# Optimization experiments

Hardware: AMD Instinct MI355X
Metric: run time of the kernel (lower is better)

Reference implementation:

```python
import jax, jax.numpy as jnp
import numpy as np

RATE = 0.999  # moving_average_rate
EPS_NORM = 1e-12
EPS_CNT = 1e-6


def l2norm(v, axis=-1):
    # matches torch F.normalize(dim=axis) with default eps
    n = jnp.sqrt(jnp.sum(v * v, axis=axis, keepdims=True))
    return v / jnp.maximum(n, EPS_NORM)


def setup_inputs() -> dict:
    key = jax.random.key(0)
    ks = jax.random.split(key, 7)
    b, c, h, w, k = 8, 256, 64, 64, 2048
    x = jax.random.normal(ks[0], (b, c, h, w), dtype=jnp.float32)
    y = jax.random.uniform(ks[1], (b, 4, h, w), dtype=jnp.float32)
    feat_w = jax.random.normal(ks[2], (k, c + 4), dtype=jnp.float32) * 0.02
    w1 = jax.random.normal(ks[3], (c + 4, c), dtype=jnp.float32) * 0.02
    b1 = jnp.zeros((c,), dtype=jnp.float32)
    w2 = jax.random.normal(ks[4], (c, c), dtype=jnp.float32) * 0.02
    b2 = jnp.zeros((c,), dtype=jnp.float32)
    return {"x": x, "y": y, "feat_w": feat_w, "w1": w1, "b1": b1, "w2": w2, "b2": b2}


def reference(x, y, feat_w, w1, b1, w2, b2):
    b, c, h, w = x.shape
    k = feat_w.shape[0]
    # flatten spatial: (n, c) with n = b*h*w
    x_flat = jnp.transpose(x, (0, 2, 3, 1)).reshape(-1, c)
    y_flat = jnp.transpose(y, (0, 2, 3, 1)).reshape(-1, 4)

    # cosine-similarity scores against codebook features (no grad in original)
    xn = l2norm(x_flat)                       # (n, c)
    mn = l2norm(feat_w[:, :-4])               # (k, c)
    score = xn @ mn.T                         # (n, k)

    # top1 EMA codebook update
    xy = jnp.concatenate([x_flat, y_flat], axis=1)          # (n, c+4)
    ind = jnp.argmax(score, axis=1)                          # (n,)
    counts = jax.ops.segment_sum(jnp.ones_like(ind, jnp.float32), ind, num_segments=k)  # (k,)
    sums = jax.ops.segment_sum(xy, ind, num_segments=k)      # (k, c+4)
    embed_mean = sums / (counts[:, None] + EPS_CNT)          # (k, c+4)
    new_w = feat_w * RATE + embed_mean * (1.0 - RATE)        # (k, c+4)

    # softmax attention over (updated) normalized codebook
    p = jax.nn.softmax(score, axis=1)                        # (n, k)
    out = p @ l2norm(new_w)                                  # (n, c+4)

    # MLP: Linear -> GELU -> Linear (drop=0)
    out = jax.nn.gelu(out @ w1 + b1) @ w2 + b2               # (n, c)
    return jnp.transpose(out.reshape(b, h, w, c), (0, 3, 1, 2))
```

## Files before the change

kernel.cpp:

```cpp
#include <hip/hip_runtime.h>
#include <cstdint>
#include <cstddef>


typedef short v8s __attribute__((ext_vector_type(8)));
typedef float v4f __attribute__((ext_vector_type(4)));

__device__ __forceinline__ unsigned short f2b(float f) {
  unsigned u = __float_as_uint(f);
  u = (u + 0x7FFFu + ((u >> 16) & 1u)) >> 16;
  return (unsigned short)u;
}
__device__ __forceinline__ float b2f(short s) {
  return __uint_as_float((unsigned)(unsigned short)s << 16);
}
__device__ __forceinline__ float gelu_t(float x) {
  float x3 = x * x * x;
  return 0.5f * x * (1.0f + tanhf(0.7978845608028654f * (x + 0.044715f * x3)));
}
__device__ __forceinline__ float gelu_fast(float x) {
  float u = 0.7978845608028654f * (x + 0.044715f * x * x * x);
  float tt = __expf(2.0f * u);
  return x * tt * __builtin_amdgcn_rcpf(tt + 1.0f);
}
__device__ __forceinline__ unsigned int mono(float f) {
  unsigned u = __float_as_uint(f);
  return (u & 0x80000000u) ? ~u : (u | 0x80000000u);
}
__device__ __forceinline__ void async16(const short* g, short* l) {
  __builtin_amdgcn_global_load_lds(
      (const __attribute__((address_space(1))) unsigned int*)g,
      (__attribute__((address_space(3))) unsigned int*)l, 16, 0, 0);
}

__global__ void transpose_norm_kernel(const float* __restrict__ x, short* __restrict__ xn,
                                      float* __restrict__ norms) {
  __shared__ float tile[32 * 257];
  __shared__ float part[8][32];
  __shared__ float invn[32];
  int t = threadIdx.x, bx = blockIdx.x;
  int b = bx >> 7, st = bx & 127;
  int s0 = st * 32;
  int sl = t & 31, cp = t >> 5;
  const float* xb = x + (size_t)b * 256 * 4096 + s0 + sl;
  float ss = 0.f;
#pragma unroll 4
  for (int i = 0; i < 32; ++i) {
    int c = cp * 32 + i;
    float v = xb[(size_t)c * 4096];
    tile[sl * 257 + c] = v;
    ss += v * v;
  }
  part[cp][sl] = ss;
  __syncthreads();
  if (t < 32) {
    float tot = 0.f;
#pragma unroll
    for (int p = 0; p < 8; ++p) tot += part[p][t];
    float nrm = fmaxf(sqrtf(tot), 1e-12f);
    invn[t] = 1.0f / nrm;
    norms[(size_t)b * 4096 + s0 + t] = nrm;
  }
  __syncthreads();
  size_t obase = ((size_t)b * 4096 + s0) * 256 + t;
  for (int s = 0; s < 32; ++s)
    xn[obase + (size_t)s * 256] = (short)f2b(tile[s * 257 + t] * invn[s]);
}

__global__ void cbnorm_kernel(const float* __restrict__ fw, short* __restrict__ mn) {
  int t = threadIdx.x;
  int wv = t >> 6, l = t & 63;
  int r = blockIdx.x * 4 + wv;
  const float* row = fw + (size_t)r * 260;
  float v[4]; float ss = 0.f;
#pragma unroll
  for (int p = 0; p < 4; ++p) { v[p] = row[l + p * 64]; ss += v[p] * v[p]; }
#pragma unroll
  for (int m = 1; m < 64; m <<= 1) ss += __shfl_xor(ss, m, 64);
  float inv = 1.0f / fmaxf(sqrtf(ss), 1e-12f);
#pragma unroll
  for (int p = 0; p < 4; ++p) mn[(size_t)r * 256 + l + p * 64] = (short)f2b(v[p] * inv);
}

template <int KTOT, int LDA, int LDB>
__device__ __forceinline__ void gemm_core2(const short* __restrict__ A, const short* __restrict__ B,
                                           int mt, int nt, int t, v4f acc[4][4],
                                           short* smem) {
  short* As = smem;
  short* Bs = smem + 4096;
  const int l = t & 63, w = t >> 6;
  const int wm = w >> 1, wn = w & 1;
  const int lane16 = l & 15, q4 = l >> 4;
#pragma unroll
  for (int i = 0; i < 4; ++i)
#pragma unroll
    for (int j = 0; j < 4; ++j)
#pragma unroll
      for (int r = 0; r < 4; ++r) acc[i][j][r] = 0.0f;
  const int srow = (w << 5) + (l >> 2);
  const int scol = (l & 3) << 3;
  const short* ga = A + (size_t)(mt * 128 + srow) * LDA + scol;
  const short* gb = B + (size_t)(nt * 128 + srow) * LDB + scol;
  short* la = As + (w << 5) * 32;
  short* lb = Bs + (w << 5) * 32;
  int kk = 0;
  for (; kk + 64 <= KTOT; kk += 64) {
    async16(ga + kk, la);
    async16(ga + (size_t)16 * LDA + kk, la + 512);
    async16(gb + kk, lb);
    async16(gb + (size_t)16 * LDB + kk, lb + 512);
    async16(ga + kk + 32, la + 8192);
    async16(ga + (size_t)16 * LDA + kk + 32, la + 8704);
    async16(gb + kk + 32, lb + 8192);
    async16(gb + (size_t)16 * LDB + kk + 32, lb + 8704);
    __syncthreads();
    v8s af[4], bf[4];
#pragma unroll
    for (int i = 0; i < 4; ++i) af[i] = *(const v8s*)&As[(wm * 64 + i * 16 + lane16) * 32 + q4 * 8];
#pragma unroll
    for (int j = 0; j < 4; ++j) bf[j] = *(const v8s*)&Bs[(wn * 64 + j * 16 + lane16) * 32 + q4 * 8];
#pragma unroll
    for (int i = 0; i < 4; ++i)
#pragma unroll
      for (int j = 0; j < 4; ++j)
        acc[i][j] = __builtin_amdgcn_mfma_f32_16x16x32_bf16(af[i], bf[j], acc[i][j], 0, 0, 0);
#pragma unroll
    for (int i = 0; i < 4; ++i) af[i] = *(const v8s*)&As[8192 + (wm * 64 + i * 16 + lane16) * 32 + q4 * 8];
#pragma unroll
    for (int j = 0; j < 4; ++j) bf[j] = *(const v8s*)&Bs[8192 + (wn * 64 + j * 16 + lane16) * 32 + q4 * 8];
#pragma unroll
    for (int i = 0; i < 4; ++i)
#pragma unroll
      for (int j = 0; j < 4; ++j)
        acc[i][j] = __builtin_amdgcn_mfma_f32_16x16x32_bf16(af[i], bf[j], acc[i][j], 0, 0, 0);
    __syncthreads();
  }
  if (kk < KTOT) {
    async16(ga + kk, la);
    async16(ga + (size_t)16 * LDA + kk, la + 512);
    async16(gb + kk, lb);
    async16(gb + (size_t)16 * LDB + kk, lb + 512);
    __syncthreads();
    v8s af[4], bf[4];
#pragma unroll
    for (int i = 0; i < 4; ++i) af[i] = *(const v8s*)&As[(wm * 64 + i * 16 + lane16) * 32 + q4 * 8];
#pragma unroll
    for (int j = 0; j < 4; ++j) bf[j] = *(const v8s*)&Bs[(wn * 64 + j * 16 + lane16) * 32 + q4 * 8];
#pragma unroll
    for (int i = 0; i < 4; ++i)
#pragma unroll
      for (int j = 0; j < 4; ++j)
        acc[i][j] = __builtin_amdgcn_mfma_f32_16x16x32_bf16(af[i], bf[j], acc[i][j], 0, 0, 0);
    __syncthreads();
  }
}

#define CP 136

__global__ __launch_bounds__(256, 2) void gemm1_kernel(const short* __restrict__ A, const short* __restrict__ B,
                                                       short* __restrict__ Q,
                                                       unsigned long long* __restrict__ packed_part,
                                                       float* __restrict__ lrow_part) {
  __shared__ __align__(16) short smem[18432];
  __shared__ unsigned long long partk[128][2];
  __shared__ float partq[128][2];
  int t = threadIdx.x, bx = blockIdx.x;
  int nt = bx >> 8, mt = bx & 255;
  v4f acc[4][4];
  gemm_core2<256, 256, 256>(A, B, mt, nt, t, acc, smem);
  int l = t & 63, w = t >> 6, wm = w >> 1, wn = w & 1, lane16 = l & 15, q4 = l >> 4;
  int rowbase = mt * 128, colbase = nt * 128;
#pragma unroll
  for (int i = 0; i < 4; ++i) {
#pragma unroll
    for (int r = 0; r < 4; ++r) {
      int lr = wm * 64 + i * 16 + q4 * 4 + r;
      float qs = 0.f;
      unsigned long long best = 0ull;
#pragma unroll
      for (int j = 0; j < 4; ++j) {
        float s = acc[i][j][r];
        int col_l = wn * 64 + j * 16 + lane16;
        float qv = __expf(s) - 1.0f;
        smem[lr * CP + col_l] = (short)f2b(qv);
        qs += qv;
        unsigned long long key = ((unsigned long long)mono(s) << 32) |
                                 (unsigned long long)(unsigned int)(~(unsigned)(colbase + col_l));
        if (key > best) best = key;
      }
#pragma unroll
      for (int m = 1; m < 16; m <<= 1) {
        unsigned long long ob = __shfl_xor(best, m, 64);
        if (ob > best) best = ob;
        qs += __shfl_xor(qs, m, 64);
      }
      if (lane16 == 0) { partk[lr][wn] = best; partq[lr][wn] = qs; }
    }
  }
  __syncthreads();
  if (t < 128) {
    unsigned long long b0 = partk[t][0], b1 = partk[t][1];
    packed_part[((size_t)nt << 15) + rowbase + t] = (b1 > b0) ? b1 : b0;
    lrow_part[((size_t)nt << 15) + rowbase + t] = partq[t][0] + partq[t][1];
  }
#pragma unroll
  for (int k2 = 0; k2 < 8; ++k2) {
    int idx = k2 * 256 + t;
    int row = idx >> 4, c8 = (idx & 15) * 8;
    *(v8s*)&Q[(size_t)(rowbase + row) * 2048 + colbase + c8] =
        *(const v8s*)&smem[row * CP + c8];
  }
}

__global__ void ind_kernel(const unsigned long long* __restrict__ packed_part,
                           const float* __restrict__ lrow_part,
                           int* __restrict__ ind, float* __restrict__ lrow,
                           float* __restrict__ cnt) {
  int i = blockIdx.x * 256 + threadIdx.x;
  unsigned long long best = 0ull;
  float ls = 0.f;
#pragma unroll
  for (int nt = 0; nt < 16; ++nt) {
    unsigned long long v = packed_part[((size_t)nt << 15) + i];
    if (v > best) best = v;
    ls += lrow_part[((size_t)nt << 15) + i];
  }
  int id = (int)(~(unsigned int)(best & 0xFFFFFFFFull));
  ind[i] = id;
  lrow[i] = ls;
  atomicAdd(&cnt[id], 1.0f);
}

__global__ void scan_kernel(const float* __restrict__ cnt, int* __restrict__ offs,
                            int* __restrict__ cursor) {
  __shared__ int part[256];
  int t = threadIdx.x;
  int local[8]; int s = 0;
#pragma unroll
  for (int i = 0; i < 8; ++i) { local[i] = s; s += (int)cnt[t * 8 + i]; }
  part[t] = s;
  __syncthreads();
  for (int off = 1; off < 256; off <<= 1) {
    int v = (t >= off) ? part[t - off] : 0;
    __syncthreads();
    part[t] += v;
    __syncthreads();
  }
  int base = (t > 0) ? part[t - 1] : 0;
#pragma unroll
  for (int i = 0; i < 8; ++i) {
    int o = base + local[i];
    offs[t * 8 + i] = o;
    cursor[t * 8 + i] = o;
  }
  if (t == 255) offs[2048] = part[255];
}

__global__ void fill_kernel(const int* __restrict__ ind, int* __restrict__ cursor,
                            int* __restrict__ sorted) {
  int i = blockIdx.x * 256 + threadIdx.x;
  int id = ind[i];
  int pos = atomicAdd(&cursor[id], 1);
  sorted[pos] = i;
}

__global__ void segsum_kernel(const short* __restrict__ xn, const float* __restrict__ norms,
                              const float* __restrict__ y, const int* __restrict__ offs,
                              const int* __restrict__ sorted, float* __restrict__ sums) {
  int r = blockIdx.x, t = threadIdx.x;
  int beg = offs[r], end = offs[r + 1];
  float a0 = 0.f, a1 = 0.f;
  for (int j = beg; j < end; ++j) {
    int node = sorted[j];
    float nm = norms[node];
    a0 += b2f(xn[(size_t)node * 256 + t]) * nm;
    if (t < 4) {
      int b = node >> 12, s = node & 4095;
      a1 += y[(size_t)b * 16384 + t * 4096 + s];
    }
  }
  sums[(size_t)r * 260 + t] = a0;
  if (t < 4) sums[(size_t)r * 260 + 256 + t] = a1;
}

__global__ void neww_kernel(const float* __restrict__ fw, const float* __restrict__ sums,
                            const float* __restrict__ cnt, short* __restrict__ nwt,
                            float* __restrict__ colsum) {
  int r = blockIdx.x;
  int l = threadIdx.x;
  float cv = cnt[r] + 1e-6f;
  float vals[5]; float ss = 0.f;
#pragma unroll
  for (int p = 0; p < 5; ++p) {
    int c = l + p * 64;
    float v = 0.f;
    if (c < 260) {
      float m = sums[(size_t)r * 260 + c] / cv;
      v = fw[(size_t)r * 260 + c] * 0.999f + m * 0.001f;
    }
    vals[p] = v; ss += v * v;
  }
#pragma unroll
  for (int m = 1; m < 64; m <<= 1) ss += __shfl_xor(ss, m, 64);
  float inv = 1.0f / fmaxf(sqrtf(ss), 1e-12f);
#pragma unroll
  for (int p = 0; p < 5; ++p) {
    int c = l + p * 64;
    if (c < 260) {
      float v = vals[p] * inv;
      nwt[(size_t)c * 2048 + r] = (short)f2b(v);
      atomicAdd(&colsum[c], v);
    }
  }
}

__global__ void const_kernel(const float* __restrict__ colsum, const float* __restrict__ w1,
                             const float* __restrict__ b1, const float* __restrict__ w2,
                             const float* __restrict__ b2, float* __restrict__ c0,
                             float* __restrict__ zc, float* __restrict__ hc,
                             float* __restrict__ oc) {
  __shared__ float c0s[260], hcs[256];
  int t = threadIdx.x;
  for (int c = t; c < 260; c += 256) {
    float v = colsum[c] * (1.0f / 2048.0f);
    c0s[c] = v; c0[c] = v;
  }
  __syncthreads();
  float z = b1[t];
  for (int i = 0; i < 260; ++i) z = fmaf(c0s[i], w1[(size_t)i * 256 + t], z);
  float h = gelu_t(z);
  zc[t] = z; hc[t] = h; hcs[t] = h;
  __syncthreads();
  float o = b2[t];
  for (int i = 0; i < 256; ++i) o = fmaf(hcs[i], w2[(size_t)i * 256 + t], o);
  oc[t] = o;
}

__global__ void wtrans_kernel(const float* __restrict__ w1, const float* __restrict__ w2,
                              short* __restrict__ w1t, short* __restrict__ w2t) {
  int j = blockIdx.x;
  int t = threadIdx.x;
  if (j < 256) {
    for (int i = t; i < 288; i += 64)
      w1t[(size_t)j * 288 + i] = (short)f2b(i < 260 ? w1[(size_t)i * 256 + j] : 0.0f);
  } else {
    int jj = j - 256;
    for (int i = t; i < 256; i += 64)
      w2t[(size_t)jj * 256 + i] = (short)f2b(w2[(size_t)i * 256 + jj]);
  }
}

__global__ __launch_bounds__(256, 2) void gemm2_kernel(const short* __restrict__ A, const short* __restrict__ B,
                                                       const float* __restrict__ lrow,
                                                       const float* __restrict__ colsum,
                                                       const float* __restrict__ c0,
                                                       short* __restrict__ D) {
  __shared__ __align__(16) short smem[18432];
  int t = threadIdx.x, bx = blockIdx.x;
  int nt = bx >> 8, mt = bx & 255;
  v4f acc[4][4];
  gemm_core2<2048, 2048, 2048>(A, B, mt, nt, t, acc, smem);
  int l = t & 63, w = t >> 6, wm = w >> 1, wn = w & 1, lane16 = l & 15, q4 = l >> 4;
  int rowbase = mt * 128, colbase = nt * 128;
#pragma unroll
  for (int i = 0; i < 4; ++i) {
#pragma unroll
    for (int r = 0; r < 4; ++r) {
      int lr = wm * 64 + i * 16 + q4 * 4 + r;
      float linv = 1.0f / (2048.0f + lrow[rowbase + lr]);
#pragma unroll
      for (int j = 0; j < 4; ++j) {
        int col_l = wn * 64 + j * 16 + lane16;
        int col_g = colbase + col_l;
        float v = 0.0f;
        if (col_g < 260)
          v = (colsum[col_g] + acc[i][j][r]) * linv - c0[col_g];
        smem[lr * CP + col_l] = (short)f2b(v);
      }
    }
  }
  __syncthreads();
#pragma unroll
  for (int k2 = 0; k2 < 8; ++k2) {
    int idx = k2 * 256 + t;
    int row = idx >> 4, c8 = (idx & 15) * 8;
    int cc = colbase + c8;
    if (cc < 288)
      *(v8s*)&D[(size_t)(rowbase + row) * 288 + cc] =
          *(const v8s*)&smem[row * CP + c8];
  }
}

__global__ __launch_bounds__(256, 2) void gemm3_kernel(const short* __restrict__ A, const short* __restrict__ B,
                                                       const float* __restrict__ zc,
                                                       const float* __restrict__ hc,
                                                       short* __restrict__ E) {
  __shared__ __align__(16) short smem[18432];
  int t = threadIdx.x, bx = blockIdx.x;
  int nt = bx >> 8, mt = bx & 255;
  v4f acc[4][4];
  gemm_core2<288, 288, 288>(A, B, mt, nt, t, acc, smem);
  int l = t & 63, w = t >> 6, wm = w >> 1, wn = w & 1, lane16 = l & 15, q4 = l >> 4;
  int rowbase = mt * 128, colbase = nt * 128;
#pragma unroll
  for (int i = 0; i < 4; ++i)
#pragma unroll
    for (int r = 0; r < 4; ++r) {
      int lr = wm * 64 + i * 16 + q4 * 4 + r;
#pragma unroll
      for (int j = 0; j < 4; ++j) {
        int col_l = wn * 64 + j * 16 + lane16;
        int col_g = colbase + col_l;
        float z = zc[col_g] + acc[i][j][r];
        smem[lr * CP + col_l] = (short)f2b(gelu_fast(z) - hc[col_g]);
      }
    }
  __syncthreads();
#pragma unroll
  for (int k2 = 0; k2 < 8; ++k2) {
    int idx = k2 * 256 + t;
    int row = idx >> 4, c8 = (idx & 15) * 8;
    *(v8s*)&E[(size_t)(rowbase + row) * 256 + colbase + c8] =
        *(const v8s*)&smem[row * CP + c8];
  }
}

__global__ __launch_bounds__(256, 2) void gemm4_kernel(const short* __restrict__ A, const short* __restrict__ B,
                                                       const float* __restrict__ oc,
                                                       float* __restrict__ out) {
  __shared__ __align__(16) short smem[18432];
  float* F = (float*)smem;
  int t = threadIdx.x, bx = blockIdx.x;
  int nt = bx >> 8, mt = bx & 255;
  v4f acc[4][4];
  gemm_core2<256, 256, 256>(A, B, mt, nt, t, acc, smem);
  int l = t & 63, w = t >> 6, wm = w >> 1, wn = w & 1, lane16 = l & 15, q4 = l >> 4;
  int b_ = mt >> 5;
  int sbase = (mt & 31) * 128;
  for (int q = 0; q < 4; ++q) {
    __syncthreads();
    if (wn == (q >> 1)) {
#pragma unroll
      for (int i = 0; i < 4; ++i)
#pragma unroll
        for (int r = 0; r < 4; ++r) {
          int srow = wm * 64 + i * 16 + q4 * 4 + r;
#pragma unroll
          for (int jj = 0; jj < 2; ++jj) {
            int j = (q & 1) * 2 + jj;
            int c_in = jj * 16 + lane16;
            int col_g = nt * 128 + q * 32 + c_in;
            F[c_in * 132 + srow] = oc[col_g] + acc[i][j][r];
          }
        }
    }
    __syncthreads();
#pragma unroll
    for (int k2 = 0; k2 < 4; ++k2) {
      int idx = k2 * 256 + t;
      int c_loc = idx >> 5, s4 = (idx & 31) * 4;
      v4f vv = *(const v4f*)&F[c_loc * 132 + s4];
      int cg = nt * 128 + q * 32 + c_loc;
      *(v4f*)&out[(size_t)b_ * 1048576 + (size_t)cg * 4096 + sbase + s4] = vv;
    }
  }
}

extern "C" void kernel_launch(void* const* d_in, const int* in_sizes, int n_in,
                              void* d_out, int out_size, void* d_ws, size_t ws_size,
                              hipStream_t stream) {
  const float* x  = (const float*)d_in[0];
  const float* y  = (const float*)d_in[1];
  const float* fw = (const float*)d_in[2];
  const float* w1 = (const float*)d_in[3];
  const float* b1 = (const float*)d_in[4];
  const float* w2 = (const float*)d_in[5];
  const float* b2 = (const float*)d_in[6];
  float* out = (float*)d_out;
  char* ws = (char*)d_ws;

  short* qbuf = (short*)(ws + 0);
  short* xn   = (short*)(ws + 134217728);
  short* ebuf = xn;
  short* mn   = (short*)(ws + 150994944);
  float* lrow = (float*)(ws + 152305664);
  int*   ind  = (int*)(ws + 152436736);
  float* cnt  = (float*)(ws + 152567808);
  float* sums = (float*)(ws + 152576000);
  float* lrow_part = (float*)(ws + 152576000);
  short* nwt  = (short*)(ws + 154705920);
  float* colsum = (float*)(ws + 156278784);
  float* c0   = (float*)(ws + 156279936);
  float* zc   = (float*)(ws + 156281088);
  float* hc   = (float*)(ws + 156282112);
  float* oc   = (float*)(ws + 156283136);
  short* w1t  = (short*)(ws + 156284160);
  short* w2t  = (short*)(ws + 156431616);
  short* dbuf = (short*)(ws + 156562688);
  float* norms  = (float*)(ws + 156562688);
  int*   offs   = (int*)(ws + 156693760);
  int*   cursor = (int*)(ws + 156702464);
  int*   sorted = (int*)(ws + 156710656);
  unsigned long long* packed_part =
      (unsigned long long*)(ws + 156841728);
  if (ws_size < 175437056ull) return;

  hipMemsetAsync(cnt,    0, 8192, stream);
  hipMemsetAsync(nwt,    0, 1572864, stream);
  hipMemsetAsync(colsum, 0, 1152, stream);

  transpose_norm_kernel<<<1024, 256, 0, stream>>>(x, xn, norms);
  cbnorm_kernel<<<512, 256, 0, stream>>>(fw, mn);
  gemm1_kernel<<<4096, 256, 0, stream>>>(xn, mn, qbuf, packed_part, lrow_part);
  ind_kernel<<<128, 256, 0, stream>>>(packed_part, lrow_part, ind, lrow, cnt);
  scan_kernel<<<1, 256, 0, stream>>>(cnt, offs, cursor);
  fill_kernel<<<128, 256, 0, stream>>>(ind, cursor, sorted);
  segsum_kernel<<<2048, 256, 0, stream>>>(xn, norms, y, offs, sorted, sums);
  neww_kernel<<<2048, 64, 0, stream>>>(fw, sums, cnt, nwt, colsum);
  const_kernel<<<1, 256, 0, stream>>>(colsum, w1, b1, w2, b2, c0, zc, hc, oc);
  wtrans_kernel<<<512, 64, 0, stream>>>(w1, w2, w1t, w2t);
  gemm2_kernel<<<768, 256, 0, stream>>>(qbuf, nwt, lrow, colsum, c0, dbuf);
  gemm3_kernel<<<512, 256, 0, stream>>>(dbuf, w1t, zc, hc, ebuf);
  gemm4_kernel<<<512, 256, 0, stream>>>(ebuf, w2t, oc, out);
}
```

Baseline: 403.9 us.

## Fuse score recompute, exp and P@V into flash-style attention kernel

gemm1 is cut down to computing only the per-row argmax keys, so it no longer writes the 128MB bf16 exp-score matrix or row sums. A new attn_kernel recomputes the score tiles per 64-row block, applies exp-1, accumulates row sums, and multiplies by the updated codebook in registers, replacing gemm2's read of the Q buffer. This trades the large HBM write and read for doing the first GEMM twice. It also adds lower occupancy and a serial loop over 16 column tiles with several barriers per step.

```diff
diff --git a/kernel.cpp b/kernel.cpp
--- a/kernel.cpp
+++ b/kernel.cpp
@@ -157,13 +157,10 @@
 
 #define CP 136
 
-__global__ __launch_bounds__(256, 2) void gemm1_kernel(const short* __restrict__ A, const short* __restrict__ B,
-                                                       short* __restrict__ Q,
-                                                       unsigned long long* __restrict__ packed_part,
-                                                       float* __restrict__ lrow_part) {
-  __shared__ __align__(16) short smem[18432];
+__global__ __launch_bounds__(256, 4) void gemm1_kernel(const short* __restrict__ A, const short* __restrict__ B,
+                                                       unsigned long long* __restrict__ packed_part) {
+  __shared__ __align__(16) short smem[16384];
   __shared__ unsigned long long partk[128][2];
-  __shared__ float partq[128][2];
   int t = threadIdx.x, bx = blockIdx.x;
   int nt = bx >> 8, mt = bx & 255;
   v4f acc[4][4];
@@ -175,59 +172,41 @@
 #pragma unroll
     for (int r = 0; r < 4; ++r) {
       int lr = wm * 64 + i * 16 + q4 * 4 + r;
-      float qs = 0.f;
       unsigned long long best = 0ull;
 #pragma unroll
       for (int j = 0; j < 4; ++j) {
         float s = acc[i][j][r];
-        int col_l = wn * 64 + j * 16 + lane16;
-        float qv = __expf(s) - 1.0f;
-        smem[lr * CP + col_l] = (short)f2b(qv);
-        qs += qv;
+        int col_g = colbase + wn * 64 + j * 16 + lane16;
         unsigned long long key = ((unsigned long long)mono(s) << 32) |
-                                 (unsigned long long)(unsigned int)(~(unsigned)(colbase + col_l));
+                                 (unsigned long long)(unsigned int)(~(unsigned)col_g);
         if (key > best) best = key;
       }
 #pragma unroll
       for (int m = 1; m < 16; m <<= 1) {
         unsigned long long ob = __shfl_xor(best, m, 64);
         if (ob > best) best = ob;
-        qs += __shfl_xor(qs, m, 64);
-      }
-      if (lane16 == 0) { partk[lr][wn] = best; partq[lr][wn] = qs; }
+      }
+      if (lane16 == 0) partk[lr][wn] = best;
     }
   }
   __syncthreads();
   if (t < 128) {
     unsigned long long b0 = partk[t][0], b1 = partk[t][1];
     packed_part[((size_t)nt << 15) + rowbase + t] = (b1 > b0) ? b1 : b0;
-    lrow_part[((size_t)nt << 15) + rowbase + t] = partq[t][0] + partq[t][1];
-  }
-#pragma unroll
-  for (int k2 = 0; k2 < 8; ++k2) {
-    int idx = k2 * 256 + t;
-    int row = idx >> 4, c8 = (idx & 15) * 8;
-    *(v8s*)&Q[(size_t)(rowbase + row) * 2048 + colbase + c8] =
-        *(const v8s*)&smem[row * CP + c8];
   }
 }
 
 __global__ void ind_kernel(const unsigned long long* __restrict__ packed_part,
-                           const float* __restrict__ lrow_part,
-                           int* __restrict__ ind, float* __restrict__ lrow,
-                           float* __restrict__ cnt) {
+                           int* __restrict__ ind, float* __restrict__ cnt) {
   int i = blockIdx.x * 256 + threadIdx.x;
   unsigned long long best = 0ull;
-  float ls = 0.f;
 #pragma unroll
   for (int nt = 0; nt < 16; ++nt) {
     unsigned long long v = packed_part[((size_t)nt << 15) + i];
     if (v > best) best = v;
-    ls += lrow_part[((size_t)nt << 15) + i];
   }
   int id = (int)(~(unsigned int)(best & 0xFFFFFFFFull));
   ind[i] = id;
-  lrow[i] = ls;
   atomicAdd(&cnt[id], 1.0f);
 }
 
@@ -350,44 +329,141 @@
   }
 }
 
-__global__ __launch_bounds__(256, 2) void gemm2_kernel(const short* __restrict__ A, const short* __restrict__ B,
-                                                       const float* __restrict__ lrow,
-                                                       const float* __restrict__ colsum,
-                                                       const float* __restrict__ c0,
-                                                       short* __restrict__ D) {
-  __shared__ __align__(16) short smem[18432];
-  int t = threadIdx.x, bx = blockIdx.x;
-  int nt = bx >> 8, mt = bx & 255;
-  v4f acc[4][4];
-  gemm_core2<2048, 2048, 2048>(A, B, mt, nt, t, acc, smem);
-  int l = t & 63, w = t >> 6, wm = w >> 1, wn = w & 1, lane16 = l & 15, q4 = l >> 4;
-  int rowbase = mt * 128, colbase = nt * 128;
-#pragma unroll
-  for (int i = 0; i < 4; ++i) {
+__global__ __launch_bounds__(256, 2) void attn_kernel(const short* __restrict__ xn,
+                                                      const short* __restrict__ mn,
+                                                      const short* __restrict__ nwt,
+                                                      const float* __restrict__ colsum,
+                                                      const float* __restrict__ c0,
+                                                      short* __restrict__ D) {
+  __shared__ __align__(16) short smem[32768];
+  __shared__ float lsum[64];
+  int t = threadIdx.x, mt = blockIdx.x;
+  int l = t & 63, w = t >> 6;
+  int lane16 = l & 15, q4 = l >> 4;
+  if (t < 64) lsum[t] = 0.f;
+  v4f acc_o[4][5];
+#pragma unroll
+  for (int rt = 0; rt < 4; ++rt)
+#pragma unroll
+    for (int j = 0; j < 5; ++j)
+#pragma unroll
+      for (int r = 0; r < 4; ++r) acc_o[rt][j][r] = 0.0f;
+  float qs_acc[4][4];
+#pragma unroll
+  for (int rt = 0; rt < 4; ++rt)
+#pragma unroll
+    for (int r = 0; r < 4; ++r) qs_acc[rt][r] = 0.0f;
+  const int lrow4 = l >> 2, lc8 = (l & 3) << 3;
+
+  for (int nt = 0; nt < 16; ++nt) {
+    __syncthreads();
+    v4f acc_s[4][2];
+#pragma unroll
+    for (int rt = 0; rt < 4; ++rt)
+#pragma unroll
+      for (int ct = 0; ct < 2; ++ct)
+#pragma unroll
+        for (int r = 0; r < 4; ++r) acc_s[rt][ct][r] = 0.0f;
+    for (int kh = 0; kh < 2; ++kh) {
+#pragma unroll
+      for (int s = 0; s < 4; ++s)
+        async16(xn + (size_t)(mt * 64 + s * 16 + lrow4) * 256 + kh * 128 + w * 32 + lc8,
+                &smem[w * 2048 + s * 512]);
+#pragma unroll
+      for (int s = 0; s < 8; ++s)
+        async16(mn + (size_t)(nt * 128 + s * 16 + lrow4) * 256 + kh * 128 + w * 32 + lc8,
+                &smem[8192 + w * 4096 + s * 512]);
+      __syncthreads();
+#pragma unroll
+      for (int ks = 0; ks < 4; ++ks) {
+        v8s a[4], b[2];
+#pragma unroll
+        for (int rt = 0; rt < 4; ++rt)
+          a[rt] = *(const v8s*)&smem[ks * 2048 + rt * 512 + lane16 * 32 + q4 * 8];
+#pragma unroll
+        for (int ct = 0; ct < 2; ++ct)
+          b[ct] = *(const v8s*)&smem[8192 + ks * 4096 + (2 * w + ct) * 512 + lane16 * 32 + q4 * 8];
+#pragma unroll
+        for (int rt = 0; rt < 4; ++rt)
+#pragma unroll
+          for (int ct = 0; ct < 2; ++ct)
+            acc_s[rt][ct] = __builtin_amdgcn_mfma_f32_16x16x32_bf16(a[rt], b[ct], acc_s[rt][ct], 0, 0, 0);
+      }
+      __syncthreads();
+    }
+#pragma unroll
+    for (int rt = 0; rt < 4; ++rt)
+#pragma unroll
+      for (int ct = 0; ct < 2; ++ct)
+#pragma unroll
+        for (int r = 0; r < 4; ++r) {
+          float qv = __expf(acc_s[rt][ct][r]) - 1.0f;
+          qs_acc[rt][r] += qv;
+          smem[24576 + w * 2048 + rt * 512 + (q4 * 4 + r) * 32 + ct * 16 + lane16] = (short)f2b(qv);
+        }
+    __syncthreads();
+    for (int h = 0; h < 2; ++h) {
+      int idbase = w * 10;
+#pragma unroll
+      for (int u = 0; u < 10; ++u) {
+        int id = idbase + u;
+        int ks2 = (id >= 20) ? 1 : 0;
+        int slab = id - ks2 * 20;
+        async16(nwt + (size_t)(slab * 16 + lrow4) * 2048 + nt * 128 + h * 64 + ks2 * 32 + lc8,
+                &smem[ks2 * 10240 + slab * 512]);
+      }
+      __syncthreads();
+#pragma unroll
+      for (int ks2 = 0; ks2 < 2; ++ks2) {
+        int kg = h * 2 + ks2;
+        v8s a[4], b[5];
+#pragma unroll
+        for (int rt = 0; rt < 4; ++rt)
+          a[rt] = *(const v8s*)&smem[24576 + kg * 2048 + rt * 512 + lane16 * 32 + q4 * 8];
+#pragma unroll
+        for (int j = 0; j < 5; ++j)
+          b[j] = *(const v8s*)&smem[ks2 * 10240 + (w * 5 + j) * 512 + lane16 * 32 + q4 * 8];
+#pragma unroll
+        for (int rt = 0; rt < 4; ++rt)
+#pragma unroll
+          for (int j = 0; j < 5; ++j)
+            acc_o[rt][j] = __builtin_amdgcn_mfma_f32_16x16x32_bf16(a[rt], b[j], acc_o[rt][j], 0, 0, 0);
+      }
+      __syncthreads();
+    }
+  }
+#pragma unroll
+  for (int rt = 0; rt < 4; ++rt)
 #pragma unroll
     for (int r = 0; r < 4; ++r) {
-      int lr = wm * 64 + i * 16 + q4 * 4 + r;
-      float linv = 1.0f / (2048.0f + lrow[rowbase + lr]);
-#pragma unroll
-      for (int j = 0; j < 4; ++j) {
-        int col_l = wn * 64 + j * 16 + lane16;
-        int col_g = colbase + col_l;
-        float v = 0.0f;
-        if (col_g < 260)
-          v = (colsum[col_g] + acc[i][j][r]) * linv - c0[col_g];
-        smem[lr * CP + col_l] = (short)f2b(v);
-      }
-    }
-  }
-  __syncthreads();
-#pragma unroll
-  for (int k2 = 0; k2 < 8; ++k2) {
+      float v = qs_acc[rt][r];
+#pragma unroll
+      for (int m = 1; m < 16; m <<= 1) v += __shfl_xor(v, m, 64);
+      if (lane16 == 0) atomicAdd(&lsum[rt * 16 + q4 * 4 + r], v);
+    }
+  __syncthreads();
+#pragma unroll
+  for (int rt = 0; rt < 4; ++rt)
+#pragma unroll
+    for (int r = 0; r < 4; ++r) {
+      int m = rt * 16 + q4 * 4 + r;
+      float linv = 1.0f / (2048.0f + lsum[m]);
+#pragma unroll
+      for (int j = 0; j < 5; ++j) {
+        int c = w * 80 + j * 16 + lane16;
+        if (c < 288) {
+          float v = 0.0f;
+          if (c < 260) v = (colsum[c] + acc_o[rt][j][r]) * linv - c0[c];
+          smem[m * 296 + c] = (short)f2b(v);
+        }
+      }
+    }
+  __syncthreads();
+#pragma unroll
+  for (int k2 = 0; k2 < 9; ++k2) {
     int idx = k2 * 256 + t;
-    int row = idx >> 4, c8 = (idx & 15) * 8;
-    int cc = colbase + c8;
-    if (cc < 288)
-      *(v8s*)&D[(size_t)(rowbase + row) * 288 + cc] =
-          *(const v8s*)&smem[row * CP + c8];
+    int row = idx / 36, ch = idx - row * 36;
+    *(v8s*)&D[(size_t)(mt * 64 + row) * 288 + ch * 8] = *(const v8s*)&smem[row * 296 + ch * 8];
   }
 }
 
@@ -479,31 +555,28 @@
   float* out = (float*)d_out;
   char* ws = (char*)d_ws;
 
-  short* qbuf = (short*)(ws + 0);
-  short* xn   = (short*)(ws + 134217728);
-  short* ebuf = xn;
-  short* mn   = (short*)(ws + 150994944);
-  float* lrow = (float*)(ws + 152305664);
-  int*   ind  = (int*)(ws + 152436736);
-  float* cnt  = (float*)(ws + 152567808);
-  float* sums = (float*)(ws + 152576000);
-  float* lrow_part = (float*)(ws + 152576000);
-  short* nwt  = (short*)(ws + 154705920);
-  float* colsum = (float*)(ws + 156278784);
-  float* c0   = (float*)(ws + 156279936);
-  float* zc   = (float*)(ws + 156281088);
-  float* hc   = (float*)(ws + 156282112);
-  float* oc   = (float*)(ws + 156283136);
-  short* w1t  = (short*)(ws + 156284160);
-  short* w2t  = (short*)(ws + 156431616);
-  short* dbuf = (short*)(ws + 156562688);
-  float* norms  = (float*)(ws + 156562688);
-  int*   offs   = (int*)(ws + 156693760);
-  int*   cursor = (int*)(ws + 156702464);
-  int*   sorted = (int*)(ws + 156710656);
+  short* xn   = (short*)(ws + 0);
+  short* mn   = (short*)(ws + 16777216);
   unsigned long long* packed_part =
-      (unsigned long long*)(ws + 156841728);
-  if (ws_size < 175437056ull) return;
+      (unsigned long long*)(ws + 17825792);
+  int*   ind  = (int*)(ws + 22020096);
+  float* cnt  = (float*)(ws + 22151168);
+  float* sums = (float*)(ws + 22159360);
+  short* nwt  = (short*)(ws + 24289280);
+  float* colsum = (float*)(ws + 25862144);
+  float* c0   = (float*)(ws + 25863296);
+  float* zc   = (float*)(ws + 25864448);
+  float* hc   = (float*)(ws + 25865472);
+  float* oc   = (float*)(ws + 25866496);
+  short* w1t  = (short*)(ws + 25867520);
+  short* w2t  = (short*)(ws + 26014976);
+  short* dbuf = (short*)(ws + 26148864);
+  short* ebuf = (short*)(ws + 45023232);
+  float* norms  = (float*)(ws + 61800448);
+  int*   offs   = (int*)(ws + 61931520);
+  int*   cursor = (int*)(ws + 61940224);
+  int*   sorted = (int*)(ws + 61948416);
+  if (ws_size < 62079488ull) return;
 
   hipMemsetAsync(cnt,    0, 8192, stream);
   hipMemsetAsync(nwt,    0, 1572864, stream);
@@ -511,15 +584,15 @@
 
   transpose_norm_kernel<<<1024, 256, 0, stream>>>(x, xn, norms);
   cbnorm_kernel<<<512, 256, 0, stream>>>(fw, mn);
-  gemm1_kernel<<<4096, 256, 0, stream>>>(xn, mn, qbuf, packed_part, lrow_part);
-  ind_kernel<<<128, 256, 0, stream>>>(packed_part, lrow_part, ind, lrow, cnt);
+  gemm1_kernel<<<4096, 256, 0, stream>>>(xn, mn, packed_part);
+  ind_kernel<<<128, 256, 0, stream>>>(packed_part, ind, cnt);
   scan_kernel<<<1, 256, 0, stream>>>(cnt, offs, cursor);
   fill_kernel<<<128, 256, 0, stream>>>(ind, cursor, sorted);
   segsum_kernel<<<2048, 256, 0, stream>>>(xn, norms, y, offs, sorted, sums);
   neww_kernel<<<2048, 64, 0, stream>>>(fw, sums, cnt, nwt, colsum);
   const_kernel<<<1, 256, 0, stream>>>(colsum, w1, b1, w2, b2, c0, zc, hc, oc);
   wtrans_kernel<<<512, 64, 0, stream>>>(w1, w2, w1t, w2t);
-  gemm2_kernel<<<768, 256, 0, stream>>>(qbuf, nwt, lrow, colsum, c0, dbuf);
+  attn_kernel<<<512, 256, 0, stream>>>(xn, mn, nwt, colsum, c0, dbuf);
   gemm3_kernel<<<512, 256, 0, stream>>>(dbuf, w1t, zc, hc, ebuf);
   gemm4_kernel<<<512, 256, 0, stream>>>(ebuf, w2t, oc, out);
 }
```

Result: slower. 425.2 us (+5.3%).
